# Kernel tuning notes

Measured on AMD Instinct MI355X. Metric: run time of the kernel, lower is better.

## Reference

```python
import jax, jax.numpy as jnp
import numpy as np

EMBED = 1024
HEAD = 64
NHEADS = EMBED // HEAD  # 16
EPS = 1e-5


def layernorm(x, g, b):
    m = jnp.mean(x, axis=-1, keepdims=True)
    v = jnp.var(x, axis=-1, keepdims=True)
    return (x - m) * jax.lax.rsqrt(v + EPS) * g + b


def msa(x, Wq, Wk, Wv):
    # x: [B,T,C]; Wq/Wk/Wv: [H, C, hd] (per-head, no bias)
    B, T, C = x.shape
    q = jnp.einsum('btc,hcd->bhtd', x, Wq)
    k = jnp.einsum('btc,hcd->bhtd', x, Wk)
    v = jnp.einsum('btc,hcd->bhtd', x, Wv)
    # NOTE: source scales by embed_size C ** -0.5, not head_size
    wei = jnp.einsum('bhtd,bhsd->bhts', q, k) * (C ** -0.5)
    wei = jax.nn.softmax(wei, axis=-1)
    out = jnp.einsum('bhts,bhsd->bhtd', wei, v)
    # concat heads (head order matches torch ModuleList cat)
    return out.transpose(0, 2, 1, 3).reshape(B, T, C)


def setup_inputs() -> dict:
    key = jax.random.key(0)
    ks = jax.random.split(key, 12)
    B, T, C = 4, 1024, EMBED
    s = C ** -0.5
    inp = {
        'x': jax.random.normal(ks[0], (B, T, C), jnp.float32),
        'Wq1': jax.random.normal(ks[1], (NHEADS, C, HEAD), jnp.float32) * s,
        'Wk1': jax.random.normal(ks[2], (NHEADS, C, HEAD), jnp.float32) * s,
        'Wv1': jax.random.normal(ks[3], (NHEADS, C, HEAD), jnp.float32) * s,
        'Wq2': jax.random.normal(ks[4], (NHEADS, C, HEAD), jnp.float32) * s,
        'Wk2': jax.random.normal(ks[5], (NHEADS, C, HEAD), jnp.float32) * s,
        'Wv2': jax.random.normal(ks[6], (NHEADS, C, HEAD), jnp.float32) * s,
        'g1': jnp.ones((C,), jnp.float32), 'b1': jnp.zeros((C,), jnp.float32),
        'g2': jnp.ones((C,), jnp.float32), 'b2': jnp.zeros((C,), jnp.float32),
        'g3': jnp.ones((C,), jnp.float32), 'b3': jnp.zeros((C,), jnp.float32),
        'W1': jax.random.normal(ks[7], (C, 4 * C), jnp.float32) * s,
        'bf1': jnp.zeros((4 * C,), jnp.float32),
        'W2': jax.random.normal(ks[8], (4 * C, C), jnp.float32) * (4 * C) ** -0.5,
        'bf2': jnp.zeros((C,), jnp.float32),
    }
    return inp


def reference(x, Wq1, Wk1, Wv1, Wq2, Wk2, Wv2, g1, b1, g2, b2, g3, b3, W1, bf1, W2, bf2):
    x = x + msa(layernorm(x, g1, b1), Wq1, Wk1, Wv1)
    x = x + msa(layernorm(x, g2, b2), Wq2, Wk2, Wv2)
    h = layernorm(x, g3, b3)
    h = jax.nn.relu(h @ W1 + bf1) @ W2 + bf2
    return x + h
```

## Files before the change

kernel.cpp:

```cpp
#include <hip/hip_runtime.h>


#define DEVI __device__ __forceinline__

typedef unsigned short u16;
typedef short bf16x8 __attribute__((ext_vector_type(8)));
typedef float f32x4 __attribute__((ext_vector_type(4)));
typedef unsigned short u16x4 __attribute__((ext_vector_type(4)));

DEVI u16 f2bf(float f) {
  union { float f; unsigned u; } v; v.f = f;
  unsigned r = v.u + 0x7FFFu + ((v.u >> 16) & 1u);
  return (u16)(r >> 16);
}
DEVI float bf2f(u16 u) {
  union { unsigned u; float f; } v; v.u = ((unsigned)u) << 16; return v.f;
}

DEVI void gload16(const void* g, void* l) {
  __builtin_amdgcn_global_load_lds((const __attribute__((address_space(1))) void*)g,
                                   (__attribute__((address_space(3))) void*)l,
                                   16, 0, 0);
}


__global__ __launch_bounds__(256) void k_pack_headw(const float* __restrict__ W,
                                                    u16* __restrict__ out) {
  const int k0 = blockIdx.x * 64;
  const int h  = blockIdx.y;
  __shared__ float t[64][65];
  const int tid = threadIdx.x;
#pragma unroll
  for (int p = 0; p < 16; p++) {
    int e = p * 256 + tid, kk = e >> 6, d = e & 63;
    t[kk][d] = W[h * 65536 + (k0 + kk) * 64 + d];
  }
  __syncthreads();
#pragma unroll
  for (int p = 0; p < 16; p++) {
    int e = p * 256 + tid, d = e >> 6, kk = e & 63;
    out[(size_t)(h * 64 + d) * 1024 + k0 + kk] = f2bf(t[kk][d]);
  }
}

__global__ __launch_bounds__(256) void k_transpose(const float* __restrict__ in,
                                                   u16* __restrict__ out,
                                                   int R, int C) {
  const int c0 = blockIdx.x * 64, r0 = blockIdx.y * 64;
  __shared__ float t[64][65];
  const int tid = threadIdx.x;
#pragma unroll
  for (int p = 0; p < 16; p++) {
    int e = p * 256 + tid, rr = e >> 6, cc = e & 63;
    t[rr][cc] = in[(size_t)(r0 + rr) * C + c0 + cc];
  }
  __syncthreads();
#pragma unroll
  for (int p = 0; p < 16; p++) {
    int e = p * 256 + tid, cc = e >> 6, rr = e & 63;
    out[(size_t)(c0 + cc) * R + r0 + rr] = f2bf(t[rr][cc]);
  }
}

__global__ __launch_bounds__(256) void k_ln(const float* __restrict__ xin,
                                            const u16* __restrict__ oin,
                                            float* __restrict__ xsum,
                                            u16* __restrict__ xn,
                                            const float* __restrict__ g,
                                            const float* __restrict__ b) {
  const int row = blockIdx.x;
  const size_t base = (size_t)row * 1024;
  const int tid = threadIdx.x;
  float4 xv = ((const float4*)(xin + base))[tid];
  if (oin) {
    u16x4 ov = *(const u16x4*)(oin + base + tid * 4);
    xv.x += bf2f(ov[0]); xv.y += bf2f(ov[1]);
    xv.z += bf2f(ov[2]); xv.w += bf2f(ov[3]);
  }
  if (xsum) ((float4*)(xsum + base))[tid] = xv;
  float s = xv.x + xv.y + xv.z + xv.w;
  float q = xv.x * xv.x + xv.y * xv.y + xv.z * xv.z + xv.w * xv.w;
#pragma unroll
  for (int m = 1; m < 64; m <<= 1) { s += __shfl_xor(s, m); q += __shfl_xor(q, m); }
  __shared__ float red[8];
  const int wave = tid >> 6, lane = tid & 63;
  if (lane == 0) { red[wave] = s; red[4 + wave] = q; }
  __syncthreads();
  s = red[0] + red[1] + red[2] + red[3];
  q = red[4] + red[5] + red[6] + red[7];
  const float mean = s * (1.f / 1024.f);
  const float var  = q * (1.f / 1024.f) - mean * mean;
  const float rstd = rsqrtf(var + 1e-5f);
  float4 gv = ((const float4*)g)[tid];
  float4 bv = ((const float4*)b)[tid];
  u16x4 o;
  o[0] = f2bf((xv.x - mean) * rstd * gv.x + bv.x);
  o[1] = f2bf((xv.y - mean) * rstd * gv.y + bv.y);
  o[2] = f2bf((xv.z - mean) * rstd * gv.z + bv.z);
  o[3] = f2bf((xv.w - mean) * rstd * gv.w + bv.w);
  *(u16x4*)(xn + base + tid * 4) = o;
}

template <int EPI>
__global__ __launch_bounds__(256) void gemm_bt(const u16* __restrict__ A,
                                               const u16* __restrict__ Bt,
                                               void* __restrict__ outp,
                                               const float* __restrict__ bias,
                                               const float* __restrict__ resid,
                                               int M, int N, int K) {
  __shared__ u16 As[128 * 32];
  __shared__ u16 Bs[128 * 32];
  const int tid = threadIdx.x;
  const int wave = tid >> 6, lane = tid & 63;
  const int lg = lane >> 4, l15 = lane & 15;
  const int wr = wave >> 1, wc = wave & 1;
  const int by = blockIdx.y, bx = blockIdx.x;

  const u16* Ab = A + (size_t)by * 128 * K;
  const u16* Bb = Bt + (size_t)bx * 128 * K;

  const int r0 = tid >> 2, c0 = (tid & 3) * 8;
  const int r1 = (256 + tid) >> 2;
  char* lA0 = (char*)As + (wave * 64) * 16;
  char* lA1 = (char*)As + (256 + wave * 64) * 16;
  char* lB0 = (char*)Bs + (wave * 64) * 16;
  char* lB1 = (char*)Bs + (256 + wave * 64) * 16;

  const f32x4 zero = {0.f, 0.f, 0.f, 0.f};
  f32x4 acc[4][4];
#pragma unroll
  for (int i = 0; i < 4; i++)
#pragma unroll
    for (int j = 0; j < 4; j++) acc[i][j] = zero;

  for (int kk = 0; kk < K; kk += 32) {
    gload16(Ab + (size_t)r0 * K + kk + c0, lA0);
    gload16(Ab + (size_t)r1 * K + kk + c0, lA1);
    gload16(Bb + (size_t)r0 * K + kk + c0, lB0);
    gload16(Bb + (size_t)r1 * K + kk + c0, lB1);
    __syncthreads();
    bf16x8 af[4], bfv[4];
#pragma unroll
    for (int i = 0; i < 4; i++)
      af[i] = *(const bf16x8*)&As[(wr * 64 + i * 16 + l15) * 32 + lg * 8];
#pragma unroll
    for (int j = 0; j < 4; j++)
      bfv[j] = *(const bf16x8*)&Bs[(wc * 64 + j * 16 + l15) * 32 + lg * 8];
#pragma unroll
    for (int i = 0; i < 4; i++)
#pragma unroll
      for (int j = 0; j < 4; j++)
        acc[i][j] = __builtin_amdgcn_mfma_f32_16x16x32_bf16(af[i], bfv[j], acc[i][j], 0, 0, 0);
    __syncthreads();
  }

  const int rbase = by * 128 + wr * 64 + lg * 4;
  const int cbase = bx * 128 + wc * 64 + l15;
  if constexpr (EPI == 0) {
    u16* out = (u16*)outp;
#pragma unroll
    for (int i = 0; i < 4; i++)
#pragma unroll
      for (int j = 0; j < 4; j++)
#pragma unroll
        for (int r = 0; r < 4; r++)
          out[(size_t)(rbase + i * 16 + r) * N + cbase + j * 16] = f2bf(acc[i][j][r]);
  } else if constexpr (EPI == 1) {
    u16* out = (u16*)outp;
#pragma unroll
    for (int j = 0; j < 4; j++) {
      const float bv = bias[cbase + j * 16];
#pragma unroll
      for (int i = 0; i < 4; i++)
#pragma unroll
        for (int r = 0; r < 4; r++)
          out[(size_t)(rbase + i * 16 + r) * N + cbase + j * 16] =
              f2bf(fmaxf(acc[i][j][r] + bv, 0.f));
    }
  } else {
    float* out = (float*)outp;
#pragma unroll
    for (int j = 0; j < 4; j++) {
      const float bv = bias[cbase + j * 16];
#pragma unroll
      for (int i = 0; i < 4; i++)
#pragma unroll
        for (int r = 0; r < 4; r++) {
          const size_t idx = (size_t)(rbase + i * 16 + r) * N + cbase + j * 16;
          out[idx] = acc[i][j][r] + bv + resid[idx];
        }
    }
  }
}

__global__ __launch_bounds__(256) void k_packkv(const u16* __restrict__ QKV,
                                                u16* __restrict__ Kp,
                                                u16* __restrict__ Vp) {
  const int t  = blockIdx.x;
  const int bh = blockIdx.y, b = bh >> 4, h = bh & 15;
  const int tid = threadIdx.x;
  __shared__ u16 vt[64][80];

  const u16* Ksrc = QKV + (size_t)(b * 1024 + t * 64) * 3072 + 1024 + h * 64;
  const u16* Vsrc = QKV + (size_t)(b * 1024 + t * 64) * 3072 + 2048 + h * 64;
  u16* KpT = Kp + (size_t)(bh * 16 + t) * 4096;
  u16* VpT = Vp + (size_t)(bh * 16 + t) * 4096;

#pragma unroll
  for (int p = 0; p < 2; p++) {
    int e = p * 256 + tid, rr = e >> 3, dd = (e & 7) * 8;
    *(bf16x8*)&vt[rr][dd] = *(const bf16x8*)(Ksrc + (size_t)rr * 3072 + dd);
  }
  __syncthreads();
#pragma unroll
  for (int p = 0; p < 2; p++) {
    int c = p * 256 + tid;
    int i = c >> 6, lane = c & 63, lgg = lane >> 4, ll = lane & 15;
    int j = i >> 1;
    int row = 8 * (ll >> 2) + (ll & 3) + (j & 1) * 4 + (j >> 1) * 32;
    int col = (i & 1) * 32 + lgg * 8;
    *(bf16x8*)&KpT[(size_t)c * 8] = *(const bf16x8*)&vt[row][col];
  }
  __syncthreads();
#pragma unroll
  for (int p = 0; p < 2; p++) {
    int e = p * 256 + tid, rr = e >> 3, dd = (e & 7) * 8;
    *(bf16x8*)&vt[rr][dd] = *(const bf16x8*)(Vsrc + (size_t)rr * 3072 + dd);
  }
  __syncthreads();
#pragma unroll
  for (int p = 0; p < 2; p++) {
    int c = p * 256 + tid;
    int i = c >> 6, lane = c & 63, lgg = lane >> 4, ll = lane & 15;
    int dg = (i >> 1) & 3, kh = i & 1;
    bf16x8 o;
#pragma unroll
    for (int jj = 0; jj < 8; jj++)
      o[jj] = (short)vt[kh * 32 + lgg * 8 + jj][dg * 16 + ll];
    *(bf16x8*)&VpT[(size_t)c * 8] = o;
  }
}

DEVI void load8(bf16x8 (&r)[8], const u16* p) {
#pragma unroll
  for (int i = 0; i < 8; i++) r[i] = *(const bf16x8*)(p + i * 512);
}

DEVI void attn_tile32(const bf16x8 (&kr)[8], const bf16x8 (&vr)[8],
                      const bf16x8 (&qf)[2][2], f32x4 (&oa)[2][4],
                      float (&m)[2], float (&sden)[2], int lg, float cexp) {
  const f32x4 zero = {0.f, 0.f, 0.f, 0.f};
#pragma unroll
  for (int qh = 0; qh < 2; qh++) {
    f32x4 s0 = zero, s1 = zero, s2 = zero, s3 = zero;
    s0 = __builtin_amdgcn_mfma_f32_16x16x32_bf16(kr[0], qf[qh][0], s0, 0, 0, 0);
    s0 = __builtin_amdgcn_mfma_f32_16x16x32_bf16(kr[1], qf[qh][1], s0, 0, 0, 0);
    s1 = __builtin_amdgcn_mfma_f32_16x16x32_bf16(kr[2], qf[qh][0], s1, 0, 0, 0);
    s1 = __builtin_amdgcn_mfma_f32_16x16x32_bf16(kr[3], qf[qh][1], s1, 0, 0, 0);
    s2 = __builtin_amdgcn_mfma_f32_16x16x32_bf16(kr[4], qf[qh][0], s2, 0, 0, 0);
    s2 = __builtin_amdgcn_mfma_f32_16x16x32_bf16(kr[5], qf[qh][1], s2, 0, 0, 0);
    s3 = __builtin_amdgcn_mfma_f32_16x16x32_bf16(kr[6], qf[qh][0], s3, 0, 0, 0);
    s3 = __builtin_amdgcn_mfma_f32_16x16x32_bf16(kr[7], qf[qh][1], s3, 0, 0, 0);

    f32x4 mv = s0;
#pragma unroll
    for (int r = 0; r < 4; r++) mv[r] = fmaxf(fmaxf(mv[r], s1[r]), fmaxf(s2[r], s3[r]));
    float mx = fmaxf(fmaxf(mv[0], mv[1]), fmaxf(mv[2], mv[3]));
    mx = fmaxf(mx, __shfl_xor(mx, 16));
    mx = fmaxf(mx, __shfl_xor(mx, 32));
    const float mn = fmaxf(m[qh], mx);
    const float fr = exp2f((m[qh] - mn) * cexp);
    m[qh] = mn;
#pragma unroll
    for (int r = 0; r < 4; r++) {
      s0[r] = exp2f((s0[r] - mn) * cexp);
      s1[r] = exp2f((s1[r] - mn) * cexp);
      s2[r] = exp2f((s2[r] - mn) * cexp);
      s3[r] = exp2f((s3[r] - mn) * cexp);
    }
    f32x4 sv = (s0 + s1) + (s2 + s3);
    float ts = (sv[0] + sv[1]) + (sv[2] + sv[3]);
    ts += __shfl_xor(ts, 16);
    ts += __shfl_xor(ts, 32);
    sden[qh] = sden[qh] * fr + ts;

    bf16x8 pa0, pa1;
#pragma unroll
    for (int r = 0; r < 4; r++) {
      pa0[r]     = (short)f2bf(s0[r]);
      pa0[4 + r] = (short)f2bf(s1[r]);
      pa1[r]     = (short)f2bf(s2[r]);
      pa1[4 + r] = (short)f2bf(s3[r]);
    }

    float frq[4];
#pragma unroll
    for (int r = 0; r < 4; r++) frq[r] = __shfl(fr, 20 * lg + r, 64);
#pragma unroll
    for (int dg = 0; dg < 4; dg++) {
      oa[qh][dg][0] *= frq[0]; oa[qh][dg][1] *= frq[1];
      oa[qh][dg][2] *= frq[2]; oa[qh][dg][3] *= frq[3];
      oa[qh][dg] = __builtin_amdgcn_mfma_f32_16x16x32_bf16(pa0, vr[2 * dg],     oa[qh][dg], 0, 0, 0);
      oa[qh][dg] = __builtin_amdgcn_mfma_f32_16x16x32_bf16(pa1, vr[2 * dg + 1], oa[qh][dg], 0, 0, 0);
    }
  }
}

__global__ __launch_bounds__(256) void k_attn(const u16* __restrict__ QKV,
                                              const u16* __restrict__ Kp,
                                              const u16* __restrict__ Vp,
                                              u16* __restrict__ O) {
  const int Tn = 1024;
  const int bh = blockIdx.x, b = bh >> 4, h = bh & 15;
  const int q0 = blockIdx.y * 128;
  const int tid = threadIdx.x, wave = tid >> 6, lane = tid & 63;
  const int lg = lane >> 4, l15 = lane & 15;

  const u16* Qb = QKV + (size_t)(b * Tn + q0 + wave * 32 + l15) * 3072 + h * 64 + lg * 8;
  bf16x8 qf[2][2];
  qf[0][0] = *(const bf16x8*)Qb;
  qf[0][1] = *(const bf16x8*)(Qb + 32);
  qf[1][0] = *(const bf16x8*)(Qb + 16 * 3072);
  qf[1][1] = *(const bf16x8*)(Qb + 16 * 3072 + 32);

  const u16* KpB = Kp + (size_t)bh * 65536 + lane * 8;
  const u16* VpB = Vp + (size_t)bh * 65536 + lane * 8;

  const float cexp = 0.03125f * 1.44269504f;

  float m[2] = {-1e30f, -1e30f}, sden[2] = {0.f, 0.f};
  const f32x4 zero = {0.f, 0.f, 0.f, 0.f};
  f32x4 oa[2][4];
#pragma unroll
  for (int qh = 0; qh < 2; qh++)
#pragma unroll
    for (int dg = 0; dg < 4; dg++) oa[qh][dg] = zero;

  bf16x8 ka[8], va[8], kb[8], vb[8];
  load8(ka, KpB);
  load8(va, VpB);

  for (int t = 0; t < 16; t += 2) {
    load8(kb, KpB + (t + 1) * 4096);
    load8(vb, VpB + (t + 1) * 4096);
    attn_tile32(ka, va, qf, oa, m, sden, lg, cexp);
    if (t + 2 < 16) {
      load8(ka, KpB + (t + 2) * 4096);
      load8(va, VpB + (t + 2) * 4096);
    }
    attn_tile32(kb, vb, qf, oa, m, sden, lg, cexp);
  }

#pragma unroll
  for (int qh = 0; qh < 2; qh++) {
    float sdq[4];
#pragma unroll
    for (int r = 0; r < 4; r++) sdq[r] = 1.f / __shfl(sden[qh], 20 * lg + r, 64);
    u16* Ob = O + (size_t)(b * Tn + q0 + wave * 32 + qh * 16) * 1024 + h * 64;
#pragma unroll
    for (int dg = 0; dg < 4; dg++)
#pragma unroll
      for (int r = 0; r < 4; r++)
        Ob[(size_t)(lg * 4 + r) * 1024 + dg * 16 + l15] = f2bf(oa[qh][dg][r] * sdq[r]);
  }
}

extern "C" void kernel_launch(void* const* d_in, const int* in_sizes, int n_in,
                              void* d_out, int out_size, void* d_ws, size_t ws_size,
                              hipStream_t stream) {
  const float* x   = (const float*)d_in[0];
  const float* Wq1 = (const float*)d_in[1];
  const float* Wk1 = (const float*)d_in[2];
  const float* Wv1 = (const float*)d_in[3];
  const float* Wq2 = (const float*)d_in[4];
  const float* Wk2 = (const float*)d_in[5];
  const float* Wv2 = (const float*)d_in[6];
  const float* g1  = (const float*)d_in[7];
  const float* b1  = (const float*)d_in[8];
  const float* g2  = (const float*)d_in[9];
  const float* b2  = (const float*)d_in[10];
  const float* g3  = (const float*)d_in[11];
  const float* b3  = (const float*)d_in[12];
  const float* W1  = (const float*)d_in[13];
  const float* bf1 = (const float*)d_in[14];
  const float* W2  = (const float*)d_in[15];
  const float* bf2 = (const float*)d_in[16];

  char* ws = (char*)d_ws;
  u16* Wqkv1t = (u16*)(ws);
  u16* Wqkv2t = (u16*)(ws + 6291456);
  u16* W1t    = (u16*)(ws + 12582912);
  u16* W2t    = (u16*)(ws + 20971520);
  u16* xn     = (u16*)(ws + 29360128);
  u16* QKV    = (u16*)(ws + 37748736);
  u16* Kp     = (u16*)(ws + 62914560);
  u16* Vp     = (u16*)(ws + 71303168);
  u16* O      = (u16*)(ws + 79691776);
  u16* h1     = (u16*)(ws + 37748736);
  float* xacc = (float*)d_out;

  const dim3 blk(256);

  k_pack_headw<<<dim3(16, 16), blk, 0, stream>>>(Wq1, Wqkv1t);
  k_pack_headw<<<dim3(16, 16), blk, 0, stream>>>(Wk1, Wqkv1t + 1024 * 1024);
  k_pack_headw<<<dim3(16, 16), blk, 0, stream>>>(Wv1, Wqkv1t + 2048 * 1024);
  k_pack_headw<<<dim3(16, 16), blk, 0, stream>>>(Wq2, Wqkv2t);
  k_pack_headw<<<dim3(16, 16), blk, 0, stream>>>(Wk2, Wqkv2t + 1024 * 1024);
  k_pack_headw<<<dim3(16, 16), blk, 0, stream>>>(Wv2, Wqkv2t + 2048 * 1024);
  k_transpose<<<dim3(64, 16), blk, 0, stream>>>(W1, W1t, 1024, 4096);
  k_transpose<<<dim3(16, 64), blk, 0, stream>>>(W2, W2t, 4096, 1024);

  k_ln<<<4096, blk, 0, stream>>>(x, nullptr, nullptr, xn, g1, b1);
  gemm_bt<0><<<dim3(24, 32), blk, 0, stream>>>(xn, Wqkv1t, QKV, nullptr, nullptr, 4096, 3072, 1024);
  k_packkv<<<dim3(16, 64), blk, 0, stream>>>(QKV, Kp, Vp);
  k_attn<<<dim3(64, 8), blk, 0, stream>>>(QKV, Kp, Vp, O);
  k_ln<<<4096, blk, 0, stream>>>(x, O, xacc, xn, g2, b2);

  gemm_bt<0><<<dim3(24, 32), blk, 0, stream>>>(xn, Wqkv2t, QKV, nullptr, nullptr, 4096, 3072, 1024);
  k_packkv<<<dim3(16, 64), blk, 0, stream>>>(QKV, Kp, Vp);
  k_attn<<<dim3(64, 8), blk, 0, stream>>>(QKV, Kp, Vp, O);
  k_ln<<<4096, blk, 0, stream>>>(xacc, O, xacc, xn, g3, b3);

  gemm_bt<1><<<dim3(32, 32), blk, 0, stream>>>(xn, W1t, h1, bf1, nullptr, 4096, 4096, 1024);
  gemm_bt<2><<<dim3(8, 32), blk, 0, stream>>>(h1, W2t, (void*)xacc, bf2, xacc, 4096, 1024, 4096);

  (void)in_sizes; (void)n_in; (void)out_size; (void)ws_size;
}
```

Measured before the change: 492.1 us.

## Double-buffer GEMM LDS tiles, swizzle LDS layout, and split-K the FFN down-projection

The bf16 GEMM now uses two LDS buffers so the next K-tile's global-to-LDS loads are issued before computing the current tile. LDS rows are stored with an XOR swizzle to avoid bank conflicts, and occupancy is hinted with launch_bounds(256,4). The final W2 GEMM is split along K into two halves written to fp32 partial buffers placed in workspace. A new combine kernel adds both partials, the bias and the residual. This targets load latency and the low block count of the 8x32-grid GEMM. It costs extra fp32 traffic for the partials and one more kernel launch.

```diff
diff --git a/kernel.cpp b/kernel.cpp
--- a/kernel.cpp
+++ b/kernel.cpp
@@ -102,29 +102,48 @@
 }
 
 template <int EPI>
-__global__ __launch_bounds__(256) void gemm_bt(const u16* __restrict__ A,
-                                               const u16* __restrict__ Bt,
-                                               void* __restrict__ outp,
-                                               const float* __restrict__ bias,
-                                               const float* __restrict__ resid,
-                                               int M, int N, int K) {
-  __shared__ u16 As[128 * 32];
-  __shared__ u16 Bs[128 * 32];
+__global__ __launch_bounds__(256, 4) void gemm_bt(const u16* __restrict__ A,
+                                                  const u16* __restrict__ Bt,
+                                                  void* __restrict__ outp,
+                                                  void* __restrict__ outp2,
+                                                  const float* __restrict__ bias,
+                                                  int M, int N, int K) {
+  __shared__ u16 As[2][128 * 32];
+  __shared__ u16 Bs[2][128 * 32];
   const int tid = threadIdx.x;
   const int wave = tid >> 6, lane = tid & 63;
   const int lg = lane >> 4, l15 = lane & 15;
   const int wr = wave >> 1, wc = wave & 1;
   const int by = blockIdx.y, bx = blockIdx.x;
 
+  const int Ksz   = (EPI == 3) ? (K >> 1) : K;
+  const int kbase = (EPI == 3) ? (int)blockIdx.z * Ksz : 0;
+
   const u16* Ab = A + (size_t)by * 128 * K;
   const u16* Bb = Bt + (size_t)bx * 128 * K;
 
-  const int r0 = tid >> 2, c0 = (tid & 3) * 8;
-  const int r1 = (256 + tid) >> 2;
-  char* lA0 = (char*)As + (wave * 64) * 16;
-  char* lA1 = (char*)As + (256 + wave * 64) * 16;
-  char* lB0 = (char*)Bs + (wave * 64) * 16;
-  char* lB1 = (char*)Bs + (256 + wave * 64) * 16;
+  const int r0 = tid >> 2, q = tid & 3, r1 = r0 + 64;
+  const int c0s = (q ^ ((r0 >> 1) & 3)) * 8;
+  const int c1s = (q ^ ((r1 >> 1) & 3)) * 8;
+  char* const a0[2] = {(char*)As[0] + wave * 1024, (char*)As[1] + wave * 1024};
+  char* const a1[2] = {(char*)As[0] + 4096 + wave * 1024, (char*)As[1] + 4096 + wave * 1024};
+  char* const b0[2] = {(char*)Bs[0] + wave * 1024, (char*)Bs[1] + wave * 1024};
+  char* const b1[2] = {(char*)Bs[0] + 4096 + wave * 1024, (char*)Bs[1] + 4096 + wave * 1024};
+
+#define STAGE(b, kk)                                       \
+  gload16(Ab + (size_t)r0 * K + (kk) + c0s, a0[b]);        \
+  gload16(Ab + (size_t)r1 * K + (kk) + c1s, a1[b]);        \
+  gload16(Bb + (size_t)r0 * K + (kk) + c0s, b0[b]);        \
+  gload16(Bb + (size_t)r1 * K + (kk) + c1s, b1[b]);
+
+  int aoff[4], boff[4];
+#pragma unroll
+  for (int i = 0; i < 4; i++) {
+    int Ra = wr * 64 + i * 16 + l15;
+    aoff[i] = Ra * 64 + ((lg ^ ((Ra >> 1) & 3)) << 4);
+    int Rb = wc * 64 + i * 16 + l15;
+    boff[i] = Rb * 64 + ((lg ^ ((Rb >> 1) & 3)) << 4);
+  }
 
   const f32x4 zero = {0.f, 0.f, 0.f, 0.f};
   f32x4 acc[4][4];
@@ -133,26 +152,32 @@
 #pragma unroll
     for (int j = 0; j < 4; j++) acc[i][j] = zero;
 
-  for (int kk = 0; kk < K; kk += 32) {
-    gload16(Ab + (size_t)r0 * K + kk + c0, lA0);
-    gload16(Ab + (size_t)r1 * K + kk + c0, lA1);
-    gload16(Bb + (size_t)r0 * K + kk + c0, lB0);
-    gload16(Bb + (size_t)r1 * K + kk + c0, lB1);
+#define COMPUTE(b)                                                             \
+  {                                                                            \
+    bf16x8 af[4], bfv[4];                                                      \
+    _Pragma("unroll") for (int i = 0; i < 4; i++)                              \
+        af[i] = *(const bf16x8*)((const char*)As[b] + aoff[i]);                \
+    _Pragma("unroll") for (int j = 0; j < 4; j++)                              \
+        bfv[j] = *(const bf16x8*)((const char*)Bs[b] + boff[j]);               \
+    _Pragma("unroll") for (int i = 0; i < 4; i++)                              \
+        _Pragma("unroll") for (int j = 0; j < 4; j++)                          \
+            acc[i][j] = __builtin_amdgcn_mfma_f32_16x16x32_bf16(               \
+                af[i], bfv[j], acc[i][j], 0, 0, 0);                            \
+  }
+
+  const int NT = Ksz >> 5;
+  STAGE(0, kbase);
+  __syncthreads();
+  for (int t = 0; t < NT; t += 2) {
+    STAGE(1, kbase + (t + 1) * 32);
+    COMPUTE(0);
     __syncthreads();
-    bf16x8 af[4], bfv[4];
-#pragma unroll
-    for (int i = 0; i < 4; i++)
-      af[i] = *(const bf16x8*)&As[(wr * 64 + i * 16 + l15) * 32 + lg * 8];
-#pragma unroll
-    for (int j = 0; j < 4; j++)
-      bfv[j] = *(const bf16x8*)&Bs[(wc * 64 + j * 16 + l15) * 32 + lg * 8];
-#pragma unroll
-    for (int i = 0; i < 4; i++)
-#pragma unroll
-      for (int j = 0; j < 4; j++)
-        acc[i][j] = __builtin_amdgcn_mfma_f32_16x16x32_bf16(af[i], bfv[j], acc[i][j], 0, 0, 0);
+    if (t + 2 < NT) { STAGE(0, kbase + (t + 2) * 32); }
+    COMPUTE(1);
     __syncthreads();
   }
+#undef STAGE
+#undef COMPUTE
 
   const int rbase = by * 128 + wr * 64 + lg * 4;
   const int cbase = bx * 128 + wc * 64 + l15;
@@ -178,19 +203,31 @@
               f2bf(fmaxf(acc[i][j][r] + bv, 0.f));
     }
   } else {
-    float* out = (float*)outp;
-#pragma unroll
-    for (int j = 0; j < 4; j++) {
-      const float bv = bias[cbase + j * 16];
-#pragma unroll
-      for (int i = 0; i < 4; i++)
-#pragma unroll
-        for (int r = 0; r < 4; r++) {
-          const size_t idx = (size_t)(rbase + i * 16 + r) * N + cbase + j * 16;
-          out[idx] = acc[i][j][r] + bv + resid[idx];
-        }
-    }
-  }
+    float* out = blockIdx.z ? (float*)outp2 : (float*)outp;
+#pragma unroll
+    for (int i = 0; i < 4; i++)
+#pragma unroll
+      for (int j = 0; j < 4; j++)
+#pragma unroll
+        for (int r = 0; r < 4; r++)
+          out[(size_t)(rbase + i * 16 + r) * N + cbase + j * 16] = acc[i][j][r];
+  }
+}
+
+__global__ __launch_bounds__(256) void k_comb(const float* __restrict__ P0,
+                                              const float* __restrict__ P1,
+                                              const float* __restrict__ bias,
+                                              float* __restrict__ xacc) {
+  const size_t i = (size_t)blockIdx.x * 1024 + threadIdx.x * 4;
+  float4 a = *(const float4*)(P0 + i);
+  float4 b = *(const float4*)(P1 + i);
+  float4 x = *(const float4*)(xacc + i);
+  float4 bv = *(const float4*)(bias + threadIdx.x * 4);
+  x.x += a.x + b.x + bv.x;
+  x.y += a.y + b.y + bv.y;
+  x.z += a.z + b.z + bv.z;
+  x.w += a.w + b.w + bv.w;
+  *(float4*)(xacc + i) = x;
 }
 
 __global__ __launch_bounds__(256) void k_packkv(const u16* __restrict__ QKV,
@@ -397,6 +434,8 @@
   u16* Vp     = (u16*)(ws + 71303168);
   u16* O      = (u16*)(ws + 79691776);
   u16* h1     = (u16*)(ws + 37748736);
+  float* P0   = (float*)(ws);
+  float* P1   = (float*)(ws + 71303168);
   float* xacc = (float*)d_out;
 
   const dim3 blk(256);
@@ -421,8 +460,9 @@
   k_attn<<<dim3(64, 8), blk, 0, stream>>>(QKV, Kp, Vp, O);
   k_ln<<<4096, blk, 0, stream>>>(xacc, O, xacc, xn, g3, b3);
 
-  gemm_bt<1><<<dim3(32, 32), blk, 0, stream>>>(xn, W1t, h1, bf1, nullptr, 4096, 4096, 1024);
-  gemm_bt<2><<<dim3(8, 32), blk, 0, stream>>>(h1, W2t, (void*)xacc, bf2, xacc, 4096, 1024, 4096);
+  gemm_bt<1><<<dim3(32, 32), blk, 0, stream>>>(xn, W1t, h1, nullptr, bf1, 4096, 4096, 1024);
+  gemm_bt<3><<<dim3(8, 32, 2), blk, 0, stream>>>(h1, W2t, P0, P1, nullptr, 4096, 1024, 4096);
+  k_comb<<<4096, blk, 0, stream>>>(P0, P1, bf2, xacc);
 
   (void)in_sizes; (void)n_in; (void)out_size; (void)ws_size;
 }
```

After: 454.6 us. 1.08x faster.
